# Performance work log

Measured on AMD Instinct MI355X. Metric: run time of the kernel, lower is better.

## Reference

```python
import jax, jax.numpy as jnp
import numpy as np

N_EMBED = 1024
EMBED_DIM = 64
BETA = 0.25


def setup_inputs() -> dict:
    key = jax.random.key(0)
    k1, k2 = jax.random.split(key)
    x = jax.random.normal(k1, (32, EMBED_DIM, 64, 64), dtype=jnp.float32)  # NCHW, C == embed_dim
    embed = jax.random.uniform(
        k2, (N_EMBED, EMBED_DIM), dtype=jnp.float32,
        minval=-1.0 / N_EMBED, maxval=1.0 / N_EMBED,
    )
    return {"x": x, "embed": embed}


def reference(x, embed):
    # NCHW -> NHWC, flatten spatial+batch to rows of embed_dim
    z = jnp.transpose(x, (0, 2, 3, 1))                      # [B,H,W,D]
    zf = z.reshape(-1, EMBED_DIM)                           # [N,D]
    # squared L2 distance to every codeword: ||z||^2 + ||e||^2 - 2 z.e
    dist = (
        jnp.sum(zf * zf, axis=1, keepdims=True)
        + jnp.sum(embed * embed, axis=1)
        - 2.0 * zf @ embed.T
    )                                                       # [N, n_embed]
    idx = jnp.argmin(dist, axis=1)                          # [N]
    # one-hot @ embed == direct gather (same math, no scatter/matmul)
    z_q = embed[idx].reshape(z.shape)                       # [B,H,W,D]
    sg = jax.lax.stop_gradient
    loss = jnp.mean((sg(z_q) - z) ** 2) + BETA * jnp.mean((z_q - sg(z)) ** 2)
    # straight-through estimator
    z_q = z + sg(z_q - z)
    z_q = jnp.transpose(z_q, (0, 3, 1, 2))                  # back to NCHW
    return (z_q, loss)
```

## Files before the change

### kernel.cpp

```cpp
#include <hip/hip_runtime.h>


#define TOTAL_ELEMS 8388608
#define LOSS_SCALE (1.25f / 8388608.f)

typedef float  f32x4  __attribute__((ext_vector_type(4)));
typedef __bf16 bf16x8 __attribute__((ext_vector_type(8)));
typedef unsigned int u32x4 __attribute__((ext_vector_type(4)));

static __device__ __forceinline__ unsigned short f2bf(float f) {
    unsigned int u = __float_as_uint(f);
    u += 0x7FFFu + ((u >> 16) & 1u);
    return (unsigned short)(u >> 16);
}

static __device__ __forceinline__ void gload_lds16(const void* g, void* l) {
    __builtin_amdgcn_global_load_lds(
        (const __attribute__((address_space(1))) void*)g,
        (__attribute__((address_space(3))) void*)l,
        16, 0, 0);
}

__global__ void vq_prep(const float* __restrict__ embed,
                        unsigned short* __restrict__ eb,
                        float* __restrict__ c0,
                        float* __restrict__ loss_slot) {
    int t   = blockIdx.x * 256 + threadIdx.x;
    int row = t >> 2, qd = t & 3;
    const float* src = embed + row * 64 + qd * 16;
    float s = 0.f;
    unsigned short tmp[16];
#pragma unroll
    for (int i = 0; i < 4; i++) {
        f32x4 v = *(const f32x4*)(src + i * 4);
#pragma unroll
        for (int j = 0; j < 4; j++) {
            float f = v[j];
            s += f * f;
            tmp[i * 4 + j] = f2bf(f);
        }
    }
    u32x4 w0, w1;
#pragma unroll
    for (int i = 0; i < 4; i++) {
        w0[i] = (unsigned)tmp[2*i]   | ((unsigned)tmp[2*i+1] << 16);
        w1[i] = (unsigned)tmp[8+2*i] | ((unsigned)tmp[8+2*i+1] << 16);
    }
    char* dstb = (char*)eb + row * 128;
    const int sw = (row & 7) << 4;
    *(u32x4*)(dstb + ((qd * 32) ^ sw))      = w0;
    *(u32x4*)(dstb + ((qd * 32 + 16) ^ sw)) = w1;
    s += __shfl_xor(s, 1);
    s += __shfl_xor(s, 2);
    if (qd == 0) c0[row] = 0.25f - 0.5f * s;
    if (t == 0) *loss_slot = 0.f;
}

__global__ __launch_bounds__(512, 2) void vq_main(
    const float* __restrict__ x,
    const float* __restrict__ embed,
    const unsigned short* __restrict__ eb,
    const float* __restrict__ c0,
    float* __restrict__ out,
    float* __restrict__ loss) {

    __shared__ __align__(16) unsigned char cb[131072];
    __shared__ __align__(16) float c0l[1024];
    __shared__ float lpart[8];

    const int t    = threadIdx.x;
    const int wv   = t >> 6, lane = t & 63;
    const int l15  = lane & 15, lq = lane >> 4;

    const int blk = blockIdx.x;
    const int b   = blk >> 3;
    const int h0  = (blk & 7) * 8;
    const size_t xbase = (size_t)b * 262144 + (size_t)h0 * 64;

    const char* ebp = (const char*)eb;

#pragma unroll
    for (int s = 0; s < 16; s++)
        gload_lds16(ebp + wv * 16384 + s * 1024 + lane * 16,
                    &cb[wv * 16384 + s * 1024]);

    if (t < 256) *(f32x4*)(c0l + t * 4) = *(const f32x4*)(c0 + t * 4);

    float part = 0.f;
    bf16x8 bfr[4][2];
#pragma unroll
    for (int nt = 0; nt < 4; nt++) {
#pragma unroll
        for (int kh = 0; kh < 2; kh++) {
            bf16x8 bb;
#pragma unroll
            for (int j = 0; j < 8; j++) {
                float v = x[xbase + (size_t)(kh * 32 + lq * 8 + j) * 4096
                            + (size_t)wv * 64 + nt * 16 + l15];
                part += v * v;
                bb[j] = (__bf16)v;
            }
            bfr[nt][kh] = bb;
        }
    }
    __syncthreads();

    unsigned int key[4] = {0u, 0u, 0u, 0u};
    const int swz = (l15 & 7) << 4;
#pragma unroll 8
    for (int mt = 0; mt < 64; mt++) {
        const unsigned char* rp = &cb[(mt * 16 + l15) * 128];
        bf16x8 a0 = *(const bf16x8*)(rp + ((lq * 16) ^ swz));
        bf16x8 a1 = *(const bf16x8*)(rp + ((64 + lq * 16) ^ swz));
        f32x4 c0v = *(const f32x4*)(c0l + mt * 16 + lq * 4);
        const int invm = 1023 - mt * 16 - lq * 4;
#pragma unroll
        for (int nt = 0; nt < 4; nt++) {
            f32x4 acc = __builtin_amdgcn_mfma_f32_16x16x32_bf16(a0, bfr[nt][0], c0v, 0, 0, 0);
            acc = __builtin_amdgcn_mfma_f32_16x16x32_bf16(a1, bfr[nt][1], acc, 0, 0, 0);
#pragma unroll
            for (int r = 0; r < 4; r++) {
                unsigned int k2 = (__float_as_uint(acc[r]) & 0xFFFFFC00u)
                                | (unsigned int)(invm - r);
                key[nt] = key[nt] > k2 ? key[nt] : k2;
            }
        }
    }

#pragma unroll
    for (int nt = 0; nt < 4; nt++) {
        unsigned int k = key[nt];
        unsigned int o = (unsigned int)__shfl_xor((int)k, 16); k = k > o ? k : o;
        o = (unsigned int)__shfl_xor((int)k, 32);              k = k > o ? k : o;
        key[nt] = k;
        part -= 0.5f * __uint_as_float(k & 0xFFFFFC00u);
    }

    unsigned int klo = (lane & 16) ? key[1] : key[0];
    unsigned int khi = (lane & 16) ? key[3] : key[2];
    unsigned int ks  = (lane & 32) ? khi : klo;
    const int idx = 1023 - (int)(ks & 1023u);

#pragma unroll
    for (int off = 1; off < 64; off <<= 1) part += __shfl_xor(part, off);
    if (lane == 0) lpart[wv] = part;

    const float* erow = embed + idx * 64;
    float* orow = out + xbase + (size_t)wv * 64 + lane;
#pragma unroll
    for (int c4 = 0; c4 < 16; c4++) {
        f32x4 ev = *(const f32x4*)(erow + c4 * 4);
#pragma unroll
        for (int j = 0; j < 4; j++)
            orow[(size_t)(c4 * 4 + j) * 4096] = ev[j];
    }

    __syncthreads();
    if (t == 0) {
        float s = 0.f;
#pragma unroll
        for (int i = 0; i < 8; i++) s += lpart[i];
        atomicAdd(loss, (s + 256.0f) * LOSS_SCALE);
    }
}

extern "C" void kernel_launch(void* const* d_in, const int* in_sizes, int n_in,
                              void* d_out, int out_size, void* d_ws, size_t ws_size,
                              hipStream_t stream) {
    const float* x     = (const float*)d_in[0];
    const float* embed = (const float*)d_in[1];
    unsigned short* eb = (unsigned short*)d_ws;
    float* c0          = (float*)((char*)d_ws + 131072);
    float* out  = (float*)d_out;
    float* loss = out + TOTAL_ELEMS;

    vq_prep<<<16, 256, 0, stream>>>(embed, eb, c0, loss);
    vq_main<<<256, 512, 0, stream>>>(x, embed, eb, c0, out, loss);
}
```

Baseline: 39.01 us.

## Switch codebook and input distance matmul from bf16 to fp8 with finer blocking

Quantises the codebook (pre-scaled by 1024) and the input vectors to fp8 and uses fp8 MFMA for the distance computation. The bias term and the loss correction are rescaled to match. This halves the LDS codebook footprint, so launch bounds allow 4 blocks per CU, and the grid doubles to 512 blocks of 4 rows each. It is meant to cut LDS and instruction cost and raise occupancy. The risk is that fp8 precision in both operands may pick different nearest codewords and skew the loss term.

```diff
diff --git a/kernel.cpp b/kernel.cpp
--- a/kernel.cpp
+++ b/kernel.cpp
@@ -5,14 +5,7 @@
 #define LOSS_SCALE (1.25f / 8388608.f)
 
 typedef float  f32x4  __attribute__((ext_vector_type(4)));
-typedef __bf16 bf16x8 __attribute__((ext_vector_type(8)));
-typedef unsigned int u32x4 __attribute__((ext_vector_type(4)));
-
-static __device__ __forceinline__ unsigned short f2bf(float f) {
-    unsigned int u = __float_as_uint(f);
-    u += 0x7FFFu + ((u >> 16) & 1u);
-    return (unsigned short)(u >> 16);
-}
+typedef unsigned int u32x2 __attribute__((ext_vector_type(2)));
 
 static __device__ __forceinline__ void gload_lds16(const void* g, void* l) {
     __builtin_amdgcn_global_load_lds(
@@ -22,49 +15,43 @@
 }
 
 __global__ void vq_prep(const float* __restrict__ embed,
-                        unsigned short* __restrict__ eb,
+                        unsigned char* __restrict__ eb,
                         float* __restrict__ c0,
                         float* __restrict__ loss_slot) {
     int t   = blockIdx.x * 256 + threadIdx.x;
     int row = t >> 2, qd = t & 3;
     const float* src = embed + row * 64 + qd * 16;
     float s = 0.f;
-    unsigned short tmp[16];
+    unsigned int d[4];
 #pragma unroll
     for (int i = 0; i < 4; i++) {
         f32x4 v = *(const f32x4*)(src + i * 4);
-#pragma unroll
-        for (int j = 0; j < 4; j++) {
-            float f = v[j];
-            s += f * f;
-            tmp[i * 4 + j] = f2bf(f);
-        }
+        s += v[0]*v[0] + v[1]*v[1] + v[2]*v[2] + v[3]*v[3];
+        unsigned int r = 0;
+        r = __builtin_amdgcn_cvt_pk_fp8_f32(v[0] * 1024.f, v[1] * 1024.f, r, false);
+        r = __builtin_amdgcn_cvt_pk_fp8_f32(v[2] * 1024.f, v[3] * 1024.f, r, true);
+        d[i] = r;
     }
-    u32x4 w0, w1;
-#pragma unroll
-    for (int i = 0; i < 4; i++) {
-        w0[i] = (unsigned)tmp[2*i]   | ((unsigned)tmp[2*i+1] << 16);
-        w1[i] = (unsigned)tmp[8+2*i] | ((unsigned)tmp[8+2*i+1] << 16);
-    }
-    char* dstb = (char*)eb + row * 128;
-    const int sw = (row & 7) << 4;
-    *(u32x4*)(dstb + ((qd * 32) ^ sw))      = w0;
-    *(u32x4*)(dstb + ((qd * 32 + 16) ^ sw)) = w1;
+    char* dstb = (char*)eb + row * 64;
+    const int sw = (row & 7) << 3;
+    u32x2 lo = {d[0], d[1]}, hi = {d[2], d[3]};
+    *(u32x2*)(dstb + ((qd * 16) ^ sw))     = lo;
+    *(u32x2*)(dstb + ((qd * 16 + 8) ^ sw)) = hi;
     s += __shfl_xor(s, 1);
     s += __shfl_xor(s, 2);
-    if (qd == 0) c0[row] = 0.25f - 0.5f * s;
+    if (qd == 0) c0[row] = 64.f - 512.f * s;
     if (t == 0) *loss_slot = 0.f;
 }
 
-__global__ __launch_bounds__(512, 2) void vq_main(
+__global__ __launch_bounds__(512, 4) void vq_main(
     const float* __restrict__ x,
     const float* __restrict__ embed,
-    const unsigned short* __restrict__ eb,
+    const unsigned char* __restrict__ eb,
     const float* __restrict__ c0,
     float* __restrict__ out,
     float* __restrict__ loss) {
 
-    __shared__ __align__(16) unsigned char cb[131072];
+    __shared__ __align__(16) unsigned char cb[65536];
     __shared__ __align__(16) float c0l[1024];
     __shared__ float lpart[8];
 
@@ -73,51 +60,60 @@
     const int l15  = lane & 15, lq = lane >> 4;
 
     const int blk = blockIdx.x;
-    const int b   = blk >> 3;
-    const int h0  = (blk & 7) * 8;
+    const int b   = blk >> 4;
+    const int h0  = (blk & 15) * 4;
     const size_t xbase = (size_t)b * 262144 + (size_t)h0 * 64;
+    const size_t rowoff = (size_t)(wv >> 1) * 64 + (wv & 1) * 32;
 
     const char* ebp = (const char*)eb;
 
 #pragma unroll
-    for (int s = 0; s < 16; s++)
-        gload_lds16(ebp + wv * 16384 + s * 1024 + lane * 16,
-                    &cb[wv * 16384 + s * 1024]);
+    for (int s = 0; s < 8; s++)
+        gload_lds16(ebp + s * 8192 + t * 16, &cb[s * 8192 + t * 16]);
 
     if (t < 256) *(f32x4*)(c0l + t * 4) = *(const f32x4*)(c0 + t * 4);
 
     float part = 0.f;
-    bf16x8 bfr[4][2];
+    unsigned long long bfr[2][2];
 #pragma unroll
-    for (int nt = 0; nt < 4; nt++) {
+    for (int nt = 0; nt < 2; nt++) {
 #pragma unroll
         for (int kh = 0; kh < 2; kh++) {
-            bf16x8 bb;
+            unsigned int dw[2];
 #pragma unroll
-            for (int j = 0; j < 8; j++) {
-                float v = x[xbase + (size_t)(kh * 32 + lq * 8 + j) * 4096
-                            + (size_t)wv * 64 + nt * 16 + l15];
-                part += v * v;
-                bb[j] = (__bf16)v;
+            for (int p = 0; p < 2; p++) {
+                float f[4];
+#pragma unroll
+                for (int j = 0; j < 4; j++) {
+                    f[j] = x[xbase + (size_t)(kh * 32 + lq * 8 + p * 4 + j) * 4096
+                             + rowoff + nt * 16 + l15];
+                    part += f[j] * f[j];
+                }
+                unsigned int r = 0;
+                r = __builtin_amdgcn_cvt_pk_fp8_f32(f[0], f[1], r, false);
+                r = __builtin_amdgcn_cvt_pk_fp8_f32(f[2], f[3], r, true);
+                dw[p] = r;
             }
-            bfr[nt][kh] = bb;
+            bfr[nt][kh] = (unsigned long long)dw[0] | ((unsigned long long)dw[1] << 32);
         }
     }
     __syncthreads();
 
-    unsigned int key[4] = {0u, 0u, 0u, 0u};
-    const int swz = (l15 & 7) << 4;
+    unsigned int key[2] = {0u, 0u};
+    const int swz = (l15 & 7) << 3;
 #pragma unroll 8
     for (int mt = 0; mt < 64; mt++) {
-        const unsigned char* rp = &cb[(mt * 16 + l15) * 128];
-        bf16x8 a0 = *(const bf16x8*)(rp + ((lq * 16) ^ swz));
-        bf16x8 a1 = *(const bf16x8*)(rp + ((64 + lq * 16) ^ swz));
+        const unsigned char* rp = &cb[(mt * 16 + l15) * 64];
+        long a0 = *(const long*)(rp + ((lq * 8) ^ swz));
+        long a1 = *(const long*)(rp + ((32 + lq * 8) ^ swz));
         f32x4 c0v = *(const f32x4*)(c0l + mt * 16 + lq * 4);
         const int invm = 1023 - mt * 16 - lq * 4;
 #pragma unroll
-        for (int nt = 0; nt < 4; nt++) {
-            f32x4 acc = __builtin_amdgcn_mfma_f32_16x16x32_bf16(a0, bfr[nt][0], c0v, 0, 0, 0);
-            acc = __builtin_amdgcn_mfma_f32_16x16x32_bf16(a1, bfr[nt][1], acc, 0, 0, 0);
+        for (int nt = 0; nt < 2; nt++) {
+            f32x4 acc = __builtin_amdgcn_mfma_f32_16x16x32_fp8_fp8(
+                a0, (long)bfr[nt][0], c0v, 0, 0, 0);
+            acc = __builtin_amdgcn_mfma_f32_16x16x32_fp8_fp8(
+                a1, (long)bfr[nt][1], acc, 0, 0, 0);
 #pragma unroll
             for (int r = 0; r < 4; r++) {
                 unsigned int k2 = (__float_as_uint(acc[r]) & 0xFFFFFC00u)
@@ -128,27 +124,26 @@
     }
 
 #pragma unroll
-    for (int nt = 0; nt < 4; nt++) {
+    for (int nt = 0; nt < 2; nt++) {
         unsigned int k = key[nt];
         unsigned int o = (unsigned int)__shfl_xor((int)k, 16); k = k > o ? k : o;
         o = (unsigned int)__shfl_xor((int)k, 32);              k = k > o ? k : o;
         key[nt] = k;
-        part -= 0.5f * __uint_as_float(k & 0xFFFFFC00u);
+        part -= (1.f / 2048.f) * __uint_as_float(k & 0xFFFFFC00u);
     }
 
-    unsigned int klo = (lane & 16) ? key[1] : key[0];
-    unsigned int khi = (lane & 16) ? key[3] : key[2];
-    unsigned int ks  = (lane & 32) ? khi : klo;
+    unsigned int ks = ((lane >> 4) & 1) ? key[1] : key[0];
     const int idx = 1023 - (int)(ks & 1023u);
 
 #pragma unroll
     for (int off = 1; off < 64; off <<= 1) part += __shfl_xor(part, off);
     if (lane == 0) lpart[wv] = part;
 
-    const float* erow = embed + idx * 64;
-    float* orow = out + xbase + (size_t)wv * 64 + lane;
+    const int ch0 = (lane >> 5) * 32;
+    const float* erow = embed + idx * 64 + ch0;
+    float* orow = out + xbase + rowoff + (lane & 31) + (size_t)ch0 * 4096;
 #pragma unroll
-    for (int c4 = 0; c4 < 16; c4++) {
+    for (int c4 = 0; c4 < 8; c4++) {
         f32x4 ev = *(const f32x4*)(erow + c4 * 4);
 #pragma unroll
         for (int j = 0; j < 4; j++)
@@ -160,7 +155,7 @@
         float s = 0.f;
 #pragma unroll
         for (int i = 0; i < 8; i++) s += lpart[i];
-        atomicAdd(loss, (s + 256.0f) * LOSS_SCALE);
+        atomicAdd(loss, (s + 32.0f) * LOSS_SCALE);
     }
 }
 
@@ -169,11 +164,11 @@
                               hipStream_t stream) {
     const float* x     = (const float*)d_in[0];
     const float* embed = (const float*)d_in[1];
-    unsigned short* eb = (unsigned short*)d_ws;
-    float* c0          = (float*)((char*)d_ws + 131072);
+    unsigned char* eb  = (unsigned char*)d_ws;
+    float* c0          = (float*)((char*)d_ws + 65536);
     float* out  = (float*)d_out;
     float* loss = out + TOTAL_ELEMS;
 
     vq_prep<<<16, 256, 0, stream>>>(embed, eb, c0, loss);
-    vq_main<<<256, 512, 0, stream>>>(x, embed, eb, c0, out, loss);
+    vq_main<<<512, 512, 0, stream>>>(x, embed, eb, c0, out, loss);
 }
```

Result: faster. 34.75 us (-10.9%).
